# Performance work log

Measured on AMD Instinct MI355X. Metric: run time of the kernel, lower is better.

## Reference

```python
import jax, jax.numpy as jnp
import numpy as np
from jax import lax

FS = 5
BL = np.array([1.46, 1.53, 1.33], np.float32)
BA = (np.pi - np.deg2rad(np.array([122.2, 111.9, 116.2]))).astype(np.float32)
A_SIN = (BL * np.sin(BA)).astype(np.float32)   # bond_length * sin(bond_angle)
A_COS = (BL * np.cos(BA)).astype(np.float32)   # bond_length * cos(bond_angle)
INIT_POS = np.array([[-np.sqrt(0.5), np.sqrt(1.5), 0.0],
                     [-np.sqrt(2.0), 0.0, 0.0],
                     [0.0, 0.0, 0.0]], np.float32)


def _rotation(pos):
    # pos: (..., 3 points, 3 coords); builds rot with columns (m_hat, n_hat x m_hat, n_hat)
    m0 = pos[..., 1, :] - pos[..., 0, :]
    m1 = pos[..., 2, :] - pos[..., 1, :]
    m_hat = m1 / (jnp.linalg.norm(m1, axis=-1, keepdims=True) + 1e-16)
    n = jnp.cross(m0, m_hat)
    n_hat = n / (jnp.linalg.norm(n, axis=-1, keepdims=True) + 1e-16)
    c = jnp.cross(n_hat, m_hat)
    return jnp.stack([m_hat, c, n_hat], axis=-1)


def _fragment_access(indices_np, fs=FS):
    # exact translation of PositionLookup.fragment index math (host-side, int constants)
    uniq, counts = np.unique(indices_np, return_counts=True)
    pad = (counts + fs - 1) // fs * fs
    last_pad = pad - counts
    off = np.roll(last_pad, 1)
    off[0] = 0
    off = np.repeat(off, counts)
    access = np.arange(counts.sum()) + off
    return access, int(pad.sum())


def _forward(torsions, access, P):
    # to_snr: (N,3) torsions -> (N, 3 atoms, 3 coords) local spherical points
    x = jnp.broadcast_to(jnp.asarray(A_COS), torsions.shape)
    points = jnp.stack([x, jnp.cos(torsions) * A_SIN, jnp.sin(torsions) * A_SIN], axis=-1)
    # fragment: scatter residues into padded per-chain slots
    padded = jnp.zeros((P, 3, 3), points.dtype).at[access].set(points)
    F = P // FS
    atom = padded.reshape(F, FS * 3, 3)          # (F, 15, 3) local snr points
    # stage 1: 15 sequential NeRF extension steps, vectorized over fragments
    pos0 = jnp.broadcast_to(jnp.asarray(INIT_POS), (F, 3, 3))
    def step(pos, d):                            # pos (F,3,3) last 3 atoms, d (F,3)
        rot = _rotation(pos)
        new = jnp.einsum('fij,fj->fi', rot, d) + pos[:, -1]
        return jnp.concatenate([pos[:, 1:], new[:, None]], axis=1), new
    _, atoms = lax.scan(step, pos0, jnp.swapaxes(atom, 0, 1))
    local = jnp.swapaxes(atoms, 0, 1)            # (F, 15, 3) fragment-local coords
    # stage 2: stitch fragments. Original right-to-left loop == exclusive prefix
    # composition of rigid transforms T_i built from fragment i's last 3 local atoms.
    rot_all = _rotation(local[:, -3:, :])        # (F,3,3)
    t_all = local[:, -1, :]                      # (F,3)
    eye = jnp.eye(3, dtype=local.dtype)[None]
    Rs = jnp.concatenate([eye, rot_all[:-1]], axis=0)
    ts = jnp.concatenate([jnp.zeros((1, 3), local.dtype), t_all[:-1]], axis=0)
    def combine(a, b):                           # (a o b)(x) = Ra(Rb x + tb) + ta
        Ra, ta = a
        Rb, tb = b
        return jnp.einsum('fij,fjk->fik', Ra, Rb), jnp.einsum('fij,fj->fi', Ra, tb) + ta
    Rp, tp = lax.associative_scan(combine, (Rs, ts))
    glob = jnp.einsum('fij,faj->fai', Rp, local) + tp[:, None, :]
    flat = glob.reshape(-1, 3)
    flat = flat - flat[:1]
    residues = flat.reshape(-1, 3, 3)            # (P//... , 3 atoms, 3 coords)
    return residues[jnp.asarray(access)]         # stitch: (N, 3, 3)


def setup_inputs():
    key = jax.random.key(0)
    n_chains, chain_len = 512, 2050              # chain_len % 5 == 0 -> zero padding
    N = n_chains * chain_len
    k1, _ = jax.random.split(key)
    torsions = jax.random.uniform(k1, (N, 3), jnp.float32, -np.pi, np.pi)
    indices = jnp.repeat(jnp.arange(n_chains, dtype=jnp.int32), chain_len)
    return {"torsions": torsions, "indices": indices}


def reference(torsions, indices):
    access, P = _fragment_access(np.asarray(indices))
    return _forward(torsions, access, P)
```

## Files before the change

kernel.cpp:

```cpp
#include <hip/hip_runtime.h>
#include <math.h>


struct Params {
    float as0, as1, as2;
    float ac0, ac1, ac2;
    float ibl0, ibl1, ibl2;
    float upx, upy, upz;
};

struct V3 { float x, y, z; };

__device__ __forceinline__ V3 v3(float x, float y, float z) { V3 r; r.x=x; r.y=y; r.z=z; return r; }
__device__ __forceinline__ V3 vcross(V3 a, V3 b) {
    return v3(a.y*b.z - a.z*b.y, a.z*b.x - a.x*b.z, a.x*b.y - a.y*b.x);
}
__device__ __forceinline__ float vdot(V3 a, V3 b) { return a.x*b.x + a.y*b.y + a.z*b.z; }

struct Xform { float r[9]; float t[3]; };

__device__ __forceinline__ Xform xf_identity() {
    Xform x;
    x.r[0]=1.f; x.r[1]=0.f; x.r[2]=0.f;
    x.r[3]=0.f; x.r[4]=1.f; x.r[5]=0.f;
    x.r[6]=0.f; x.r[7]=0.f; x.r[8]=1.f;
    x.t[0]=0.f; x.t[1]=0.f; x.t[2]=0.f;
    return x;
}

__device__ __forceinline__ Xform xf_compose(const Xform& a, const Xform& b) {
    Xform c;
#pragma unroll
    for (int i = 0; i < 3; ++i) {
#pragma unroll
        for (int j = 0; j < 3; ++j)
            c.r[i*3+j] = a.r[i*3+0]*b.r[0*3+j] + a.r[i*3+1]*b.r[1*3+j] + a.r[i*3+2]*b.r[2*3+j];
        c.t[i] = a.r[i*3+0]*b.t[0] + a.r[i*3+1]*b.t[1] + a.r[i*3+2]*b.t[2] + a.t[i];
    }
    return c;
}

__device__ __forceinline__ Xform xf_shfl_up(const Xform& x, int off) {
    Xform y;
#pragma unroll
    for (int i = 0; i < 9; ++i) y.r[i] = __shfl_up(x.r[i], off, 64);
#pragma unroll
    for (int i = 0; i < 3; ++i) y.t[i] = __shfl_up(x.t[i], off, 64);
    return y;
}
__device__ __forceinline__ Xform xf_shfl_down(const Xform& x, int off) {
    Xform y;
#pragma unroll
    for (int i = 0; i < 9; ++i) y.r[i] = __shfl_down(x.r[i], off, 64);
#pragma unroll
    for (int i = 0; i < 3; ++i) y.t[i] = __shfl_down(x.t[i], off, 64);
    return y;
}

#define LSTRIDE 13

__device__ __forceinline__ void xf_to_lds(float* p, const Xform& x) {
#pragma unroll
    for (int i = 0; i < 9; ++i) p[i] = x.r[i];
#pragma unroll
    for (int i = 0; i < 3; ++i) p[9+i] = x.t[i];
}
__device__ __forceinline__ Xform xf_from_lds(const float* p) {
    Xform x;
#pragma unroll
    for (int i = 0; i < 9; ++i) x.r[i] = p[i];
#pragma unroll
    for (int i = 0; i < 3; ++i) x.t[i] = p[9+i];
    return x;
}

__device__ __forceinline__ void xf_store_g(float* g, const Xform& x) {
    float4* q = (float4*)g;
    q[0] = make_float4(x.r[0], x.r[1], x.r[2], x.r[3]);
    q[1] = make_float4(x.r[4], x.r[5], x.r[6], x.r[7]);
    q[2] = make_float4(x.r[8], x.t[0], x.t[1], x.t[2]);
}
__device__ __forceinline__ Xform xf_load_g(const float* g) {
    const float4* q = (const float4*)g;
    float4 a = q[0], b = q[1], c = q[2];
    Xform x;
    x.r[0]=a.x; x.r[1]=a.y; x.r[2]=a.z; x.r[3]=a.w;
    x.r[4]=b.x; x.r[5]=b.y; x.r[6]=b.z; x.r[7]=b.w;
    x.r[8]=c.x; x.t[0]=c.y; x.t[1]=c.z; x.t[2]=c.w;
    return x;
}

__device__ __forceinline__ void fast_sincos(float t, float& s, float& c) {
    const float r = t * 0.15915494309189535f;
    s = __builtin_amdgcn_sinf(r);
    c = __builtin_amdgcn_cosf(r);
}

template <bool STORE>
__device__ __forceinline__ void build_fragment(const float* __restrict__ tf, const Params& prm,
                                               V3* atoms, V3& up_o, V3& u_o, V3& p_o) {
    V3 up = v3(prm.upx, prm.upy, prm.upz);
    V3 u  = v3(1.f, 0.f, 0.f);
    V3 p  = v3(0.f, 0.f, 0.f);
    const float AS[3]  = {prm.as0,  prm.as1,  prm.as2};
    const float AC[3]  = {prm.ac0,  prm.ac1,  prm.ac2};
    const float IBL[3] = {prm.ibl0, prm.ibl1, prm.ibl2};
#pragma unroll
    for (int a = 0; a < 15; ++a) {
        const int j = a % 3;
        float s, c;
        fast_sincos(tf[a], s, c);
        V3 n = vcross(up, u);
        float il = __builtin_amdgcn_rsqf(vdot(n, n));
        V3 nh = v3(n.x*il, n.y*il, n.z*il);
        V3 cc = vcross(nh, u);
        const float dy = c * AS[j], dz = s * AS[j];
        V3 w;
        w.x = AC[j]*u.x + dy*cc.x + dz*nh.x;
        w.y = AC[j]*u.y + dy*cc.y + dz*nh.y;
        w.z = AC[j]*u.z + dy*cc.z + dz*nh.z;
        p = v3(p.x + w.x, p.y + w.y, p.z + w.z);
        up = u;
        u = v3(w.x*IBL[j], w.y*IBL[j], w.z*IBL[j]);
        if (STORE) atoms[a] = p;
    }
    up_o = up; u_o = u; p_o = p;
}

__device__ __forceinline__ Xform frag_transform(V3 up, V3 u, V3 p) {
    V3 n = vcross(up, u);
    float il = __builtin_amdgcn_rsqf(vdot(n, n));
    V3 nh = v3(n.x*il, n.y*il, n.z*il);
    V3 cc = vcross(nh, u);
    Xform T;
    T.r[0]=u.x; T.r[1]=cc.x; T.r[2]=nh.x;
    T.r[3]=u.y; T.r[4]=cc.y; T.r[5]=nh.y;
    T.r[6]=u.z; T.r[7]=cc.z; T.r[8]=nh.z;
    T.t[0]=p.x; T.t[1]=p.y; T.t[2]=p.z;
    return T;
}

__device__ __forceinline__ void wave_reduce(Xform& T) {
#pragma unroll
    for (int off = 1; off < 64; off <<= 1) {
        Xform o = xf_shfl_down(T, off);
        T = xf_compose(T, o);
    }
}

__global__ __launch_bounds__(256) void k_block_agg(const float* __restrict__ tors,
                                                   float* __restrict__ agg,
                                                   int F, Params prm) {
    __shared__ __align__(16) float tslab[256 * 15];
    __shared__ float tot[4 * LSTRIDE];
    const int tid = threadIdx.x;
    const int lane = tid & 63, w = tid >> 6;
    const int f0 = blockIdx.x * 256;
    const int nfrag = min(256, F - f0);

    if (nfrag == 256) {
        const float4* tg = (const float4*)(tors + (size_t)f0 * 15);
        float4* ts4 = (float4*)tslab;
        for (int i = tid; i < 960; i += 256) ts4[i] = tg[i];
    } else {
        const int total = nfrag * 15;
        for (int i = tid; i < total; i += 256) tslab[i] = tors[(size_t)f0 * 15 + i];
    }
    __syncthreads();

    Xform T = xf_identity();
    if (tid < nfrag) {
        V3 up, u, p;
        build_fragment<false>(&tslab[tid * 15], prm, nullptr, up, u, p);
        T = frag_transform(up, u, p);
    }
    wave_reduce(T);
    if (lane == 0) xf_to_lds(&tot[w * LSTRIDE], T);
    __syncthreads();
    if (tid == 0) {
        Xform A = xf_from_lds(&tot[0]);
#pragma unroll
        for (int j = 1; j < 4; ++j) A = xf_compose(A, xf_from_lds(&tot[j * LSTRIDE]));
        xf_store_g(agg + (size_t)blockIdx.x * 12, A);
    }
}

__global__ __launch_bounds__(256) void k_apply(const float* __restrict__ tors,
                                               const float* __restrict__ agg,
                                               float* __restrict__ out,
                                               int F, Params prm) {
    __shared__ __align__(16) float stage[256 * 45];
    __shared__ float totA[4 * LSTRIDE];
    __shared__ float totB[4 * LSTRIDE];
    __shared__ float bcast[12];
    const int tid = threadIdx.x;
    const int lane = tid & 63, w = tid >> 6;
    const int b = blockIdx.x;
    const int f0 = b * 256;
    const int nfrag = min(256, F - f0);

    if (nfrag == 256) {
        const float4* tg = (const float4*)(tors + (size_t)f0 * 15);
        float4* ts4 = (float4*)stage;
        for (int i = tid; i < 960; i += 256) ts4[i] = tg[i];
    } else {
        const int total = nfrag * 15;
        for (int i = tid; i < total; i += 256) stage[i] = tors[(size_t)f0 * 15 + i];
    }
    __syncthreads();

    V3 atoms[15];
    Xform T = xf_identity();
    V3 up, u, p;
    if (tid < nfrag) {
        build_fragment<true>(&stage[tid * 15], prm, atoms, up, u, p);
        T = frag_transform(up, u, p);
    }

    Xform R = xf_identity();
    {
        const int g = (b + 255) >> 8;
        if (g) {
            const int s = tid * g;
            const int e = min(s + g, b);
            for (int k = s; k < e; ++k) R = xf_compose(R, xf_load_g(agg + (size_t)k * 12));
        }
        wave_reduce(R);
    }
#pragma unroll
    for (int off = 1; off < 64; off <<= 1) {
        Xform o = xf_shfl_up(T, off);
        if (lane >= off) T = xf_compose(o, T);
    }
    if (lane == 0)  xf_to_lds(&totB[w * LSTRIDE], R);
    if (lane == 63) xf_to_lds(&totA[w * LSTRIDE], T);
    __syncthreads();
    if (tid == 0) {
        Xform Eb = xf_from_lds(&totB[0]);
#pragma unroll
        for (int j = 1; j < 4; ++j) Eb = xf_compose(Eb, xf_from_lds(&totB[j * LSTRIDE]));
        xf_to_lds(bcast, Eb);
    }
    __syncthreads();

    Xform E = xf_from_lds(bcast);
    for (int j = 0; j < w; ++j) E = xf_compose(E, xf_from_lds(&totA[j * LSTRIDE]));
    Xform S = xf_shfl_up(T, 1);
    if (lane > 0) E = xf_compose(E, S);

    {
        float s0, c0;
        fast_sincos(tors[0], s0, c0);
        E.t[0] -= prm.ac0;
        E.t[1] -= c0 * prm.as0;
        E.t[2] -= s0 * prm.as0;
    }

    if (tid < nfrag) {
#pragma unroll
        for (int a = 0; a < 15; ++a) {
            V3 q = atoms[a];
            float gx = E.r[0]*q.x + E.r[1]*q.y + E.r[2]*q.z + E.t[0];
            float gy = E.r[3]*q.x + E.r[4]*q.y + E.r[5]*q.z + E.t[1];
            float gz = E.r[6]*q.x + E.r[7]*q.y + E.r[8]*q.z + E.t[2];
            stage[tid*45 + a*3 + 0] = gx;
            stage[tid*45 + a*3 + 1] = gy;
            stage[tid*45 + a*3 + 2] = gz;
        }
    }
    __syncthreads();

    const size_t base = (size_t)b * 256 * 45;
    if (nfrag == 256) {
        float4* o4 = (float4*)(out + base);
        const float4* s4 = (const float4*)stage;
        for (int i = tid; i < (256 * 45) / 4; i += 256) o4[i] = s4[i];
    } else {
        const int total = nfrag * 45;
        for (int i = tid; i < total; i += 256) out[base + i] = stage[i];
    }
}

extern "C" void kernel_launch(void* const* d_in, const int* in_sizes, int n_in,
                              void* d_out, int out_size, void* d_ws, size_t ws_size,
                              hipStream_t stream) {
    const float* tors = (const float*)d_in[0];
    float* out = (float*)d_out;

    const int N = in_sizes[0] / 3;
    const int F = N / 5;
    const int nb = (F + 255) / 256;

    float* agg = (float*)d_ws;

    Params P;
    {
        const double PI = 3.14159265358979323846;
        const double deg[3] = {122.2, 111.9, 116.2};
        const double bl[3]  = {1.46, 1.53, 1.33};
        float* as_ = &P.as0; float* ac_ = &P.ac0; float* ib_ = &P.ibl0;
        for (int i = 0; i < 3; ++i) {
            double ba = PI - deg[i] * PI / 180.0;
            float baf = (float)ba;
            float blf = (float)bl[i];
            as_[i] = (float)((double)blf * sin((double)baf));
            ac_[i] = (float)((double)blf * cos((double)baf));
            ib_[i] = 1.0f / blf;
        }
        P.upx = -0.5f; P.upy = -0.8660254037844386f; P.upz = 0.f;
    }

    k_block_agg<<<nb, 256, 0, stream>>>(tors, agg, F, P);
    k_apply<<<nb, 256, 0, stream>>>(tors, agg, out, F, P);
}
```

Baseline: 98.96 us.

## Replace per-step NeRF renormalization with closed-form frame composition and halve staging LDS

Each NeRF extension step is now a closed-form update of the local frame (columns X, Y, Z) using precomputed cos/sin of the bond angle. This drops the per-step cross products and rsqrt normalizations, and only the final fragment transform is re-orthonormalized. The apply kernel keeps the sin/cos values in registers and recomputes the positions from the global frame instead of holding 15 atoms. It writes output through a 128-row LDS stage in two passes, which halves shared memory and should raise occupancy. In exchange it adds syncthreads and a second recompute pass, and the frame can drift numerically because it is not re-normalized across the 15 steps.

```diff
diff --git a/kernel.cpp b/kernel.cpp
--- a/kernel.cpp
+++ b/kernel.cpp
@@ -3,14 +3,14 @@
 
 
 struct Params {
-    float as0, as1, as2;
-    float ac0, ac1, ac2;
-    float ibl0, ibl1, ibl2;
-    float upx, upy, upz;
+    float as_[3];
+    float ac_[3];
+    float bl_[3];
+    float kA[3];
+    float kS[3];
 };
 
 struct V3 { float x, y, z; };
-
 __device__ __forceinline__ V3 v3(float x, float y, float z) { V3 r; r.x=x; r.y=y; r.z=z; return r; }
 __device__ __forceinline__ V3 vcross(V3 a, V3 b) {
     return v3(a.y*b.z - a.z*b.y, a.z*b.x - a.x*b.z, a.x*b.y - a.y*b.x);
@@ -96,47 +96,35 @@
     c = __builtin_amdgcn_cosf(r);
 }
 
-template <bool STORE>
-__device__ __forceinline__ void build_fragment(const float* __restrict__ tf, const Params& prm,
-                                               V3* atoms, V3& up_o, V3& u_o, V3& p_o) {
-    V3 up = v3(prm.upx, prm.upy, prm.upz);
-    V3 u  = v3(1.f, 0.f, 0.f);
-    V3 p  = v3(0.f, 0.f, 0.f);
-    const float AS[3]  = {prm.as0,  prm.as1,  prm.as2};
-    const float AC[3]  = {prm.ac0,  prm.ac1,  prm.ac2};
-    const float IBL[3] = {prm.ibl0, prm.ibl1, prm.ibl2};
-#pragma unroll
-    for (int a = 0; a < 15; ++a) {
-        const int j = a % 3;
-        float s, c;
-        fast_sincos(tf[a], s, c);
-        V3 n = vcross(up, u);
-        float il = __builtin_amdgcn_rsqf(vdot(n, n));
-        V3 nh = v3(n.x*il, n.y*il, n.z*il);
-        V3 cc = vcross(nh, u);
-        const float dy = c * AS[j], dz = s * AS[j];
-        V3 w;
-        w.x = AC[j]*u.x + dy*cc.x + dz*nh.x;
-        w.y = AC[j]*u.y + dy*cc.y + dz*nh.y;
-        w.z = AC[j]*u.z + dy*cc.z + dz*nh.z;
-        p = v3(p.x + w.x, p.y + w.y, p.z + w.z);
-        up = u;
-        u = v3(w.x*IBL[j], w.y*IBL[j], w.z*IBL[j]);
-        if (STORE) atoms[a] = p;
-    }
-    up_o = up; u_o = u; p_o = p;
-}
-
-__device__ __forceinline__ Xform frag_transform(V3 up, V3 u, V3 p) {
-    V3 n = vcross(up, u);
+__device__ __forceinline__ void step_compose(V3& cX, V3& cY, V3& cZ, V3& t,
+                                             float s, float c, int j, const Params& prm) {
+    const float kA = prm.kA[j], kS = prm.kS[j], BL = prm.bl_[j];
+    const float csK = c * kS, snK = s * kS, csA = c * kA, snA = s * kA;
+    V3 nX = v3(kA*cX.x + csK*cY.x + snK*cZ.x,
+               kA*cX.y + csK*cY.y + snK*cZ.y,
+               kA*cX.z + csK*cY.z + snK*cZ.z);
+    V3 nY = v3(-kS*cX.x + csA*cY.x + snA*cZ.x,
+               -kS*cX.y + csA*cY.y + snA*cZ.y,
+               -kS*cX.z + csA*cY.z + snA*cZ.z);
+    V3 nZ = v3(-s*cY.x + c*cZ.x,
+               -s*cY.y + c*cZ.y,
+               -s*cY.z + c*cZ.z);
+    t = v3(BL*nX.x + t.x, BL*nX.y + t.y, BL*nX.z + t.z);
+    cX = nX; cY = nY; cZ = nZ;
+}
+
+__device__ __forceinline__ Xform frag_transform_ortho(V3 prevX, V3 cX, V3 t) {
+    float im = __builtin_amdgcn_rsqf(vdot(cX, cX));
+    V3 mh = v3(cX.x*im, cX.y*im, cX.z*im);
+    V3 n = vcross(prevX, mh);
     float il = __builtin_amdgcn_rsqf(vdot(n, n));
     V3 nh = v3(n.x*il, n.y*il, n.z*il);
-    V3 cc = vcross(nh, u);
+    V3 cc = vcross(nh, mh);
     Xform T;
-    T.r[0]=u.x; T.r[1]=cc.x; T.r[2]=nh.x;
-    T.r[3]=u.y; T.r[4]=cc.y; T.r[5]=nh.y;
-    T.r[6]=u.z; T.r[7]=cc.z; T.r[8]=nh.z;
-    T.t[0]=p.x; T.t[1]=p.y; T.t[2]=p.z;
+    T.r[0]=mh.x; T.r[1]=cc.x; T.r[2]=nh.x;
+    T.r[3]=mh.y; T.r[4]=cc.y; T.r[5]=nh.y;
+    T.r[6]=mh.z; T.r[7]=cc.z; T.r[8]=nh.z;
+    T.t[0]=t.x;  T.t[1]=t.y;  T.t[2]=t.z;
     return T;
 }
 
@@ -146,6 +134,18 @@
         Xform o = xf_shfl_down(T, off);
         T = xf_compose(T, o);
     }
+}
+
+__device__ __forceinline__ Xform chain_transform(const float* sv, const float* cv,
+                                                 const Params& prm) {
+    V3 cX = v3(1,0,0), cY = v3(0,1,0), cZ = v3(0,0,1), t = v3(0,0,0);
+    V3 prevX = cX;
+#pragma unroll
+    for (int a = 0; a < 15; ++a) {
+        prevX = cX;
+        step_compose(cX, cY, cZ, t, sv[a], cv[a], a % 3, prm);
+    }
+    return frag_transform_ortho(prevX, cX, t);
 }
 
 __global__ __launch_bounds__(256) void k_block_agg(const float* __restrict__ tors,
@@ -170,9 +170,10 @@
 
     Xform T = xf_identity();
     if (tid < nfrag) {
-        V3 up, u, p;
-        build_fragment<false>(&tslab[tid * 15], prm, nullptr, up, u, p);
-        T = frag_transform(up, u, p);
+        float sv[15], cv[15];
+#pragma unroll
+        for (int a = 0; a < 15; ++a) fast_sincos(tslab[tid * 15 + a], sv[a], cv[a]);
+        T = chain_transform(sv, cv, prm);
     }
     wave_reduce(T);
     if (lane == 0) xf_to_lds(&tot[w * LSTRIDE], T);
@@ -189,7 +190,7 @@
                                                const float* __restrict__ agg,
                                                float* __restrict__ out,
                                                int F, Params prm) {
-    __shared__ __align__(16) float stage[256 * 45];
+    __shared__ __align__(16) float lds[128 * 45];
     __shared__ float totA[4 * LSTRIDE];
     __shared__ float totB[4 * LSTRIDE];
     __shared__ float bcast[12];
@@ -201,20 +202,20 @@
 
     if (nfrag == 256) {
         const float4* tg = (const float4*)(tors + (size_t)f0 * 15);
-        float4* ts4 = (float4*)stage;
+        float4* ts4 = (float4*)lds;
         for (int i = tid; i < 960; i += 256) ts4[i] = tg[i];
     } else {
         const int total = nfrag * 15;
-        for (int i = tid; i < total; i += 256) stage[i] = tors[(size_t)f0 * 15 + i];
-    }
-    __syncthreads();
-
-    V3 atoms[15];
+        for (int i = tid; i < total; i += 256) lds[i] = tors[(size_t)f0 * 15 + i];
+    }
+    __syncthreads();
+
+    float sv[15], cv[15];
     Xform T = xf_identity();
-    V3 up, u, p;
     if (tid < nfrag) {
-        build_fragment<true>(&stage[tid * 15], prm, atoms, up, u, p);
-        T = frag_transform(up, u, p);
+#pragma unroll
+        for (int a = 0; a < 15; ++a) fast_sincos(lds[tid * 15 + a], sv[a], cv[a]);
+        T = chain_transform(sv, cv, prm);
     }
 
     Xform R = xf_identity();
@@ -251,33 +252,43 @@
     {
         float s0, c0;
         fast_sincos(tors[0], s0, c0);
-        E.t[0] -= prm.ac0;
-        E.t[1] -= c0 * prm.as0;
-        E.t[2] -= s0 * prm.as0;
-    }
-
-    if (tid < nfrag) {
-#pragma unroll
-        for (int a = 0; a < 15; ++a) {
-            V3 q = atoms[a];
-            float gx = E.r[0]*q.x + E.r[1]*q.y + E.r[2]*q.z + E.t[0];
-            float gy = E.r[3]*q.x + E.r[4]*q.y + E.r[5]*q.z + E.t[1];
-            float gz = E.r[6]*q.x + E.r[7]*q.y + E.r[8]*q.z + E.t[2];
-            stage[tid*45 + a*3 + 0] = gx;
-            stage[tid*45 + a*3 + 1] = gy;
-            stage[tid*45 + a*3 + 2] = gz;
+        E.t[0] -= prm.ac_[0];
+        E.t[1] -= c0 * prm.as_[0];
+        E.t[2] -= s0 * prm.as_[0];
+    }
+    __syncthreads();
+
+#pragma unroll
+    for (int r = 0; r < 2; ++r) {
+        const int lo = r * 128;
+        if ((tid >> 7) == r && tid < nfrag) {
+            V3 cX = v3(E.r[0], E.r[3], E.r[6]);
+            V3 cY = v3(E.r[1], E.r[4], E.r[7]);
+            V3 cZ = v3(E.r[2], E.r[5], E.r[8]);
+            V3 t  = v3(E.t[0], E.t[1], E.t[2]);
+            const int row = tid & 127;
+#pragma unroll
+            for (int a = 0; a < 15; ++a) {
+                step_compose(cX, cY, cZ, t, sv[a], cv[a], a % 3, prm);
+                lds[row*45 + a*3 + 0] = t.x;
+                lds[row*45 + a*3 + 1] = t.y;
+                lds[row*45 + a*3 + 2] = t.z;
+            }
         }
-    }
-    __syncthreads();
-
-    const size_t base = (size_t)b * 256 * 45;
-    if (nfrag == 256) {
-        float4* o4 = (float4*)(out + base);
-        const float4* s4 = (const float4*)stage;
-        for (int i = tid; i < (256 * 45) / 4; i += 256) o4[i] = s4[i];
-    } else {
-        const int total = nfrag * 45;
-        for (int i = tid; i < total; i += 256) out[base + i] = stage[i];
+        __syncthreads();
+        const int nf = max(0, min(128, nfrag - lo));
+        if (nf > 0) {
+            const size_t base = ((size_t)f0 + lo) * 45;
+            const int total = nf * 45;
+            if ((total & 3) == 0) {
+                float4* o4 = (float4*)(out + base);
+                const float4* s4 = (const float4*)lds;
+                for (int i = tid; i < total / 4; i += 256) o4[i] = s4[i];
+            } else {
+                for (int i = tid; i < total; i += 256) out[base + i] = lds[i];
+            }
+        }
+        __syncthreads();
     }
 }
 
@@ -298,16 +309,15 @@
         const double PI = 3.14159265358979323846;
         const double deg[3] = {122.2, 111.9, 116.2};
         const double bl[3]  = {1.46, 1.53, 1.33};
-        float* as_ = &P.as0; float* ac_ = &P.ac0; float* ib_ = &P.ibl0;
         for (int i = 0; i < 3; ++i) {
-            double ba = PI - deg[i] * PI / 180.0;
-            float baf = (float)ba;
+            float baf = (float)(PI - deg[i] * PI / 180.0);
             float blf = (float)bl[i];
-            as_[i] = (float)((double)blf * sin((double)baf));
-            ac_[i] = (float)((double)blf * cos((double)baf));
-            ib_[i] = 1.0f / blf;
+            P.as_[i] = (float)((double)blf * sin((double)baf));
+            P.ac_[i] = (float)((double)blf * cos((double)baf));
+            P.bl_[i] = blf;
+            P.kA[i] = P.ac_[i] / blf;
+            P.kS[i] = P.as_[i] / blf;
         }
-        P.upx = -0.5f; P.upy = -0.8660254037844386f; P.upz = 0.f;
     }
 
     k_block_agg<<<nb, 256, 0, stream>>>(tors, agg, F, P);
```

New measurement: 98.04 us. Within noise of the previous version (-0.9%).
